# Kernel tuning notes

Hardware: AMD Instinct MI355X
Metric: run time of the kernel (lower is better)

Reference implementation:

```python
import jax, jax.numpy as jnp
import numpy as np

NUM_HEADS = 8
KEY_SIZE = 64
VALUE_SIZE = 64
NUM_GROUPS = 3 * NUM_HEADS  # 24
C = NUM_HEADS * (2 * KEY_SIZE + VALUE_SIZE)  # 1536
EPS = 1e-5


def setup_inputs() -> dict:
    key = jax.random.key(0)
    k1, k2, k3 = jax.random.split(key, 3)
    x = jax.random.normal(k1, (8, C, 32, 32), dtype=jnp.float32)
    # GroupNorm affine params (torch default ones/zeros, perturbed for non-trivial grads)
    gn_weight = 1.0 + 0.1 * jax.random.normal(k2, (C,), dtype=jnp.float32)
    gn_bias = 0.1 * jax.random.normal(k3, (C,), dtype=jnp.float32)
    return {"x": x, "gn_weight": gn_weight, "gn_bias": gn_bias}


def _group_norm(x, weight, bias):
    B, Cc, H, W = x.shape
    xg = x.reshape(B, NUM_GROUPS, -1)  # [B, G, (C/G)*H*W]
    mean = jnp.mean(xg, axis=-1, keepdims=True)
    var = jnp.var(xg, axis=-1, keepdims=True)
    xn = ((xg - mean) * jax.lax.rsqrt(var + EPS)).reshape(B, Cc, H, W)
    return xn * weight[:, None, None] + bias[:, None, None]


def reference(x, gn_weight, gn_bias):
    NH, KS, VS = NUM_HEADS, KEY_SIZE, VALUE_SIZE
    B, Cc, H, W = x.shape
    xn = _group_norm(x, gn_weight, gn_bias)
    xr = xn.reshape(B, NH, 2 * KS + VS, H * W)  # [B, NH, 2KS+VS, NK]
    k = xr[:, :, :KS]            # [B, NH, KS, NK]
    q = xr[:, :, KS:2 * KS]      # [B, NH, KS, NK]
    v = xr[:, :, 2 * KS:]        # [B, NH, VS, NK]
    # saliency = q^T @ k / sqrt(KS) -> [B, NH, NKq, NKk]
    sal = jnp.einsum('bhcq,bhck->bhqk', q, k) / jnp.sqrt(jnp.float32(KS))
    mask = jax.nn.softmax(sal, axis=-1)
    # out = v @ mask^T -> [B, NH, VS, NKq]
    out = jnp.einsum('bhvk,bhqk->bhvq', v, mask)
    return out.reshape(B, NH * VS, H, W)
```

## Files before the change

kernel.cpp:

```cpp
#include <hip/hip_runtime.h>
#include <hip/hip_bf16.h>


typedef __attribute__((ext_vector_type(8))) short bf16x8;
typedef __attribute__((ext_vector_type(4))) float f32x4;
typedef __attribute__((ext_vector_type(16))) float f32x16;
typedef unsigned short u16;
typedef unsigned int u32;

#define SM_SCALE 0.18033688f
#define SM_OFF   8.0f

__device__ __forceinline__ u32 pack2(float a, float b) {
    union { float f; u32 u; } ua, ub; ua.f = a; ub.f = b;
    return __builtin_amdgcn_perm(ub.u + 0x8000u, ua.u + 0x8000u, 0x07060302u);
}
union BB { uint4 u; bf16x8 v; };

__device__ __forceinline__ float fexp2(float x) {
#if __has_builtin(__builtin_amdgcn_exp2f)
    return __builtin_amdgcn_exp2f(x);
#else
    float r; asm("v_exp_f32 %0, %1" : "=v"(r) : "v"(x)); return r;
#endif
}

__device__ __forceinline__ f32x16 zero16() {
    f32x16 z;
#pragma unroll
    for (int i = 0; i < 16; ++i) z[i] = 0.f;
    return z;
}

__device__ __forceinline__ void swap32(u32 a, u32 b, int hi, u32& ret0, u32& ret1) {
#if __has_builtin(__builtin_amdgcn_permlane32_swap)
    (void)hi;
    auto sw = __builtin_amdgcn_permlane32_swap(a, b, false, false);
    ret0 = sw[0]; ret1 = sw[1];
#else
    u32 pa = __shfl_xor(a, 32), pb = __shfl_xor(b, 32);
    ret0 = hi ? pb : a;
    ret1 = hi ? b : pa;
#endif
}

__global__ __launch_bounds__(256) void gn_partial(const float* __restrict__ x,
                                                  float* __restrict__ partials) {
    int blk = blockIdx.x;
    const float4* p = (const float4*)(x + (size_t)blk * 8192);
    int t = threadIdx.x;
    float s1a = 0.f, s2a = 0.f, s1b = 0.f, s2b = 0.f;
#pragma unroll
    for (int i = 0; i < 8; i += 2) {
        float4 va = p[t + i * 256];
        float4 vb = p[t + (i + 1) * 256];
        s1a += va.x + va.y + va.z + va.w;
        s2a += va.x*va.x + va.y*va.y + va.z*va.z + va.w*va.w;
        s1b += vb.x + vb.y + vb.z + vb.w;
        s2b += vb.x*vb.x + vb.y*vb.y + vb.z*vb.z + vb.w*vb.w;
    }
    float s1 = s1a + s1b, s2 = s2a + s2b;
    for (int off = 32; off > 0; off >>= 1) {
        s1 += __shfl_down(s1, off);
        s2 += __shfl_down(s2, off);
    }
    __shared__ float a1[4], a2[4];
    int wave = t >> 6, lane = t & 63;
    if (lane == 0) { a1[wave] = s1; a2[wave] = s2; }
    __syncthreads();
    if (t == 0) {
        partials[blk * 2 + 0] = a1[0] + a1[1] + a1[2] + a1[3];
        partials[blk * 2 + 1] = a2[0] + a2[1] + a2[2] + a2[3];
    }
}

__device__ __forceinline__ void group_stats(const float* __restrict__ partials,
                                            int bg, float& mean, float& rstd) {
    float s1 = 0.f, s2 = 0.f;
#pragma unroll
    for (int j = 0; j < 8; ++j) {
        s1 += partials[(bg * 8 + j) * 2 + 0];
        s2 += partials[(bg * 8 + j) * 2 + 1];
    }
    mean = s1 * (1.f / 65536.f);
    float var = s2 * (1.f / 65536.f) - mean * mean;
    rstd = rsqrtf(var + 1e-5f);
}

__global__ __launch_bounds__(256, 2) void attn_fused(
    const float* __restrict__ x, const float* __restrict__ gamma,
    const float* __restrict__ beta, const float* __restrict__ partials,
    float* __restrict__ out)
{
    const int bid = blockIdx.x;
    const int qt = bid >> 6;
    const int pair = bid & 63;
    const int b = pair >> 3, h = pair & 7;
    const float* xb = x + (size_t)b * 1536 * 1024;
    const int tid = threadIdx.x;
    const int w2 = tid >> 6;
    const int lane = tid & 63;
    const int li = lane & 31;
    const int hi = lane >> 5;

    float ms[3], rs[3];
    group_stats(partials, b * 24 + 3 * h + 0, ms[0], rs[0]);
    group_stats(partials, b * 24 + 3 * h + 1, ms[1], rs[1]);
    group_stats(partials, b * 24 + 3 * h + 2, ms[2], rs[2]);

    __shared__ uint4 KT[2][512];
    __shared__ uint4 VT[2][512];

    const int sr = tid & 63;
    const int cc0 = tid >> 6;
    const int kx = sr & 7;
    const int kidx0 = sr * 8 + (cc0 ^ kx);
    const int kidx1 = sr * 8 + ((cc0 + 4) ^ kx);
    const int vidx0 = sr * 8 + ((cc0 * 2) ^ kx);
    const int vidx1 = sr * 8 + ((cc0 * 2 + 1) ^ kx);

    const float* kbase = xb + (size_t)(h * 192) * 1024 + sr;
    const float* vbase = xb + (size_t)(h * 192 + 128 + sr) * 1024 + cc0 * 16;

    const int q0 = qt * 128 + w2 * 32;
    bf16x8 bq[4];
    float dqp = 0.f;
#pragma unroll
    for (int cs = 0; cs < 4; ++cs) {
        u32 qq[4];
#pragma unroll
        for (int jp = 0; jp < 4; ++jp) {
            int c0 = cs * 16 + hi * 8 + jp * 2;
            int cgq = h * 192 + 64 + c0;
            int cgk = h * 192 + c0;
            float wq0 = gamma[cgq] * rs[1],     bq0 = beta[cgq] - ms[1] * wq0;
            float wq1 = gamma[cgq + 1] * rs[1], bq1 = beta[cgq + 1] - ms[1] * wq1;
            float wk0 = gamma[cgk] * rs[0],     bk0 = beta[cgk] - ms[0] * wk0;
            float wk1 = gamma[cgk + 1] * rs[0], bk1 = beta[cgk + 1] - ms[0] * wk1;
            float a0 = xb[(size_t)cgq * 1024 + q0 + li];
            float a1 = xb[(size_t)(cgq + 1) * 1024 + q0 + li];
            float qn0 = __builtin_fmaf(a0, wq0, bq0);
            float qn1 = __builtin_fmaf(a1, wq1, bq1);
            dqp = __builtin_fmaf(bk0, qn0, dqp);
            dqp = __builtin_fmaf(bk1, qn1, dqp);
            qq[jp] = pack2(qn0 * wk0, qn1 * wk1);
        }
        BB tb; tb.u = uint4{qq[0], qq[1], qq[2], qq[3]};
        bq[cs] = tb.v;
    }
    const float dq = dqp + __shfl_xor(dqp, 32);
    const float offq = __builtin_fmaf(dq, SM_SCALE, -SM_OFF);

    f32x16 oacc[2];
    oacc[0] = zero16(); oacc[1] = zero16();
    float lsum = 0.f;

    const int x7 = li & 7;

    float rk[16], rv[16];
#define LOAD_TILE(KT_)                                                        \
    {                                                                         \
        const float* kp = kbase + (KT_) * 64;                                 \
        _Pragma("unroll")                                                     \
        for (int u = 0; u < 16; ++u) {                                        \
            int c = ((u < 8) ? cc0 : (cc0 + 4)) * 8 + (u & 7);                \
            rk[u] = kp[(size_t)c * 1024];                                     \
        }                                                                     \
        const float* vp = vbase + (KT_) * 64;                                 \
        _Pragma("unroll")                                                     \
        for (int f = 0; f < 4; ++f) {                                         \
            float4 vq = *(const float4*)(vp + f * 4);                         \
            rv[f * 4 + 0] = vq.x; rv[f * 4 + 1] = vq.y;                       \
            rv[f * 4 + 2] = vq.z; rv[f * 4 + 3] = vq.w;                       \
        }                                                                     \
    }
#define COMMIT_TILE(BUF_)                                                     \
    {                                                                         \
        uint4 ka, kc, va, vc;                                                 \
        ka.x = pack2(rk[0], rk[1]);   ka.y = pack2(rk[2], rk[3]);             \
        ka.z = pack2(rk[4], rk[5]);   ka.w = pack2(rk[6], rk[7]);             \
        kc.x = pack2(rk[8], rk[9]);   kc.y = pack2(rk[10], rk[11]);           \
        kc.z = pack2(rk[12], rk[13]); kc.w = pack2(rk[14], rk[15]);           \
        va.x = pack2(rv[0], rv[1]);   va.y = pack2(rv[2], rv[3]);             \
        va.z = pack2(rv[4], rv[5]);   va.w = pack2(rv[6], rv[7]);             \
        vc.x = pack2(rv[8], rv[9]);   vc.y = pack2(rv[10], rv[11]);           \
        vc.z = pack2(rv[12], rv[13]); vc.w = pack2(rv[14], rv[15]);           \
        KT[BUF_][kidx0] = ka; KT[BUF_][kidx1] = kc;                           \
        VT[BUF_][vidx0] = va; VT[BUF_][vidx1] = vc;                           \
    }

    LOAD_TILE(0);
    COMMIT_TILE(0);
    __syncthreads();

#pragma unroll 2
    for (int kt = 0; kt < 16; ++kt) {
        const int cur = kt & 1;
        if (kt < 15) LOAD_TILE(kt + 1);

        BB pbv[4];
#pragma unroll
        for (int kf = 0; kf < 2; ++kf) {
            bf16x8 ak[4];
#pragma unroll
            for (int cs = 0; cs < 4; ++cs)
                ak[cs] = ((const BB*)&KT[cur][(kf * 32 + li) * 8 + ((cs * 2 + hi) ^ x7)])->v;
            f32x16 acc = zero16();
            __builtin_amdgcn_s_setprio(1);
#pragma unroll
            for (int cs = 0; cs < 4; ++cs)
                acc = __builtin_amdgcn_mfma_f32_32x32x16_bf16(ak[cs], bq[cs], acc, 0, 0, 0);
            __builtin_amdgcn_s_setprio(0);
#pragma unroll
            for (int s = 0; s < 2; ++s) {
                float p0 = fexp2(__builtin_fmaf(acc[8 * s + 0], SM_SCALE, offq));
                float p1 = fexp2(__builtin_fmaf(acc[8 * s + 1], SM_SCALE, offq));
                float p2 = fexp2(__builtin_fmaf(acc[8 * s + 2], SM_SCALE, offq));
                float p3 = fexp2(__builtin_fmaf(acc[8 * s + 3], SM_SCALE, offq));
                float p4 = fexp2(__builtin_fmaf(acc[8 * s + 4], SM_SCALE, offq));
                float p5 = fexp2(__builtin_fmaf(acc[8 * s + 5], SM_SCALE, offq));
                float p6 = fexp2(__builtin_fmaf(acc[8 * s + 6], SM_SCALE, offq));
                float p7 = fexp2(__builtin_fmaf(acc[8 * s + 7], SM_SCALE, offq));
                lsum += ((p0 + p1) + (p2 + p3)) + ((p4 + p5) + (p6 + p7));
                u32 Pa = pack2(p0, p1), Pb = pack2(p2, p3);
                u32 Pc = pack2(p4, p5), Pd = pack2(p6, p7);
                u32 w0, w1, w2m, w3;
                swap32(Pa, Pc, hi, w0, w2m);
                swap32(Pb, Pd, hi, w1, w3);
                pbv[kf * 2 + s].u = uint4{w0, w1, w2m, w3};
            }
        }

#pragma unroll
        for (int vf = 0; vf < 2; ++vf) {
            bf16x8 av[4];
#pragma unroll
            for (int ks = 0; ks < 4; ++ks)
                av[ks] = ((const BB*)&VT[cur][(vf * 32 + li) * 8 + ((ks * 2 + hi) ^ x7)])->v;
            __builtin_amdgcn_s_setprio(1);
#pragma unroll
            for (int ks = 0; ks < 4; ++ks)
                oacc[vf] = __builtin_amdgcn_mfma_f32_32x32x16_bf16(av[ks], pbv[ks].v, oacc[vf], 0, 0, 0);
            __builtin_amdgcn_s_setprio(0);
        }

        if (kt < 15) COMMIT_TILE(cur ^ 1);
        __syncthreads();
    }

    lsum += __shfl_xor(lsum, 32);
    float invl = 1.f / lsum;
    float* ob = out + (size_t)pair * 65536 + q0 + li;
#pragma unroll
    for (int vf = 0; vf < 2; ++vf)
#pragma unroll
        for (int r = 0; r < 16; ++r) {
            int v = vf * 32 + (r & 3) + 8 * (r >> 2) + 4 * hi;
            int cgv = h * 192 + 128 + v;
            float wv = gamma[cgv] * rs[2];
            float bvv = beta[cgv] - ms[2] * wv;
            ob[(size_t)v * 1024] = __builtin_fmaf(oacc[vf][r] * invl, wv, bvv);
        }
}

extern "C" void kernel_launch(void* const* d_in, const int* in_sizes, int n_in,
                              void* d_out, int out_size, void* d_ws, size_t ws_size,
                              hipStream_t stream) {
    const float* x     = (const float*)d_in[0];
    const float* gamma = (const float*)d_in[1];
    const float* beta  = (const float*)d_in[2];
    float* out = (float*)d_out;

    float* partials = (float*)d_ws;

    gn_partial<<<1536, 256, 0, stream>>>(x, partials);
    attn_fused<<<512, 256, 0, stream>>>(x, gamma, beta, partials, out);
}
```

Before: 121.0 us.

## Split key range across two 256-thread groups per block and merge partial outputs

Each block now runs 512 threads as two independent 256-thread groups. Each group processes half of the 16 key tiles with its own double-buffered LDS tiles, and the partial outputs and softmax sums are combined through shared memory at the end. This doubles the waves per block to raise latency hiding, since the grid of 512 blocks gives only about two blocks per CU. The costs are an extra LDS reduction and a barrier, doubled LDS use, and block-wide __syncthreads now coupling both groups.

```diff
diff --git a/kernel.cpp b/kernel.cpp
--- a/kernel.cpp
+++ b/kernel.cpp
@@ -87,7 +87,7 @@
     rstd = rsqrtf(var + 1e-5f);
 }
 
-__global__ __launch_bounds__(256, 2) void attn_fused(
+__global__ __launch_bounds__(512, 2) void attn_fused(
     const float* __restrict__ x, const float* __restrict__ gamma,
     const float* __restrict__ beta, const float* __restrict__ partials,
     float* __restrict__ out)
@@ -98,8 +98,10 @@
     const int b = pair >> 3, h = pair & 7;
     const float* xb = x + (size_t)b * 1536 * 1024;
     const int tid = threadIdx.x;
-    const int w2 = tid >> 6;
-    const int lane = tid & 63;
+    const int wg = tid >> 8;
+    const int t = tid & 255;
+    const int w2 = t >> 6;
+    const int lane = t & 63;
     const int li = lane & 31;
     const int hi = lane >> 5;
 
@@ -108,11 +110,10 @@
     group_stats(partials, b * 24 + 3 * h + 1, ms[1], rs[1]);
     group_stats(partials, b * 24 + 3 * h + 2, ms[2], rs[2]);
 
-    __shared__ uint4 KT[2][512];
-    __shared__ uint4 VT[2][512];
-
-    const int sr = tid & 63;
-    const int cc0 = tid >> 6;
+    __shared__ uint4 TILES[2][2][2][512];
+
+    const int sr = t & 63;
+    const int cc0 = t >> 6;
     const int kx = sr & 7;
     const int kidx0 = sr * 8 + (cc0 ^ kx);
     const int kidx1 = sr * 8 + ((cc0 + 4) ^ kx);
@@ -158,15 +159,15 @@
     const int x7 = li & 7;
 
     float rk[16], rv[16];
-#define LOAD_TILE(KT_)                                                        \
+#define LOAD_TILE(KTG_)                                                       \
     {                                                                         \
-        const float* kp = kbase + (KT_) * 64;                                 \
+        const float* kp = kbase + (KTG_) * 64;                                \
         _Pragma("unroll")                                                     \
         for (int u = 0; u < 16; ++u) {                                        \
             int c = ((u < 8) ? cc0 : (cc0 + 4)) * 8 + (u & 7);                \
             rk[u] = kp[(size_t)c * 1024];                                     \
         }                                                                     \
-        const float* vp = vbase + (KT_) * 64;                                 \
+        const float* vp = vbase + (KTG_) * 64;                                \
         _Pragma("unroll")                                                     \
         for (int f = 0; f < 4; ++f) {                                         \
             float4 vq = *(const float4*)(vp + f * 4);                         \
@@ -185,18 +186,18 @@
         va.z = pack2(rv[4], rv[5]);   va.w = pack2(rv[6], rv[7]);             \
         vc.x = pack2(rv[8], rv[9]);   vc.y = pack2(rv[10], rv[11]);           \
         vc.z = pack2(rv[12], rv[13]); vc.w = pack2(rv[14], rv[15]);           \
-        KT[BUF_][kidx0] = ka; KT[BUF_][kidx1] = kc;                           \
-        VT[BUF_][vidx0] = va; VT[BUF_][vidx1] = vc;                           \
-    }
-
-    LOAD_TILE(0);
+        TILES[wg][BUF_][0][kidx0] = ka; TILES[wg][BUF_][0][kidx1] = kc;       \
+        TILES[wg][BUF_][1][vidx0] = va; TILES[wg][BUF_][1][vidx1] = vc;       \
+    }
+
+    LOAD_TILE(wg * 8);
     COMMIT_TILE(0);
     __syncthreads();
 
 #pragma unroll 2
-    for (int kt = 0; kt < 16; ++kt) {
-        const int cur = kt & 1;
-        if (kt < 15) LOAD_TILE(kt + 1);
+    for (int kt8 = 0; kt8 < 8; ++kt8) {
+        const int cur = kt8 & 1;
+        if (kt8 < 7) LOAD_TILE(wg * 8 + kt8 + 1);
 
         BB pbv[4];
 #pragma unroll
@@ -204,7 +205,7 @@
             bf16x8 ak[4];
 #pragma unroll
             for (int cs = 0; cs < 4; ++cs)
-                ak[cs] = ((const BB*)&KT[cur][(kf * 32 + li) * 8 + ((cs * 2 + hi) ^ x7)])->v;
+                ak[cs] = ((const BB*)&TILES[wg][cur][0][(kf * 32 + li) * 8 + ((cs * 2 + hi) ^ x7)])->v;
             f32x16 acc = zero16();
             __builtin_amdgcn_s_setprio(1);
 #pragma unroll
@@ -236,7 +237,7 @@
             bf16x8 av[4];
 #pragma unroll
             for (int ks = 0; ks < 4; ++ks)
-                av[ks] = ((const BB*)&VT[cur][(vf * 32 + li) * 8 + ((ks * 2 + hi) ^ x7)])->v;
+                av[ks] = ((const BB*)&TILES[wg][cur][1][(vf * 32 + li) * 8 + ((ks * 2 + hi) ^ x7)])->v;
             __builtin_amdgcn_s_setprio(1);
 #pragma unroll
             for (int ks = 0; ks < 4; ++ks)
@@ -244,23 +245,37 @@
             __builtin_amdgcn_s_setprio(0);
         }
 
-        if (kt < 15) COMMIT_TILE(cur ^ 1);
+        if (kt8 < 7) COMMIT_TILE(cur ^ 1);
         __syncthreads();
     }
 
     lsum += __shfl_xor(lsum, 32);
-    float invl = 1.f / lsum;
-    float* ob = out + (size_t)pair * 65536 + q0 + li;
-#pragma unroll
-    for (int vf = 0; vf < 2; ++vf)
-#pragma unroll
-        for (int r = 0; r < 16; ++r) {
-            int v = vf * 32 + (r & 3) + 8 * (r >> 2) + 4 * hi;
-            int cgv = h * 192 + 128 + v;
-            float wv = gamma[cgv] * rs[2];
-            float bvv = beta[cgv] - ms[2] * wv;
-            ob[(size_t)v * 1024] = __builtin_fmaf(oacc[vf][r] * invl, wv, bvv);
-        }
+    float* Osh = (float*)TILES;
+    float* lsh = Osh + 256 * 33;
+    if (wg == 1) {
+#pragma unroll
+        for (int vf = 0; vf < 2; ++vf)
+#pragma unroll
+            for (int r = 0; r < 16; ++r)
+                Osh[t * 33 + vf * 16 + r] = oacc[vf][r];
+        lsh[t] = lsum;
+    }
+    __syncthreads();
+    if (wg == 0) {
+        float invl = 1.f / (lsum + lsh[t]);
+        float* ob = out + (size_t)pair * 65536 + q0 + li;
+#pragma unroll
+        for (int vf = 0; vf < 2; ++vf)
+#pragma unroll
+            for (int r = 0; r < 16; ++r) {
+                int v = vf * 32 + (r & 3) + 8 * (r >> 2) + 4 * hi;
+                int cgv = h * 192 + 128 + v;
+                float wv = gamma[cgv] * rs[2];
+                float bvv = beta[cgv] - ms[2] * wv;
+                float o = (oacc[vf][r] + Osh[t * 33 + vf * 16 + r]) * invl;
+                ob[(size_t)v * 1024] = __builtin_fmaf(o, wv, bvv);
+            }
+    }
 }
 
 extern "C" void kernel_launch(void* const* d_in, const int* in_sizes, int n_in,
@@ -274,5 +289,5 @@
     float* partials = (float*)d_ws;
 
     gn_partial<<<1536, 256, 0, stream>>>(x, partials);
-    attn_fused<<<512, 256, 0, stream>>>(x, gamma, beta, partials, out);
-}
+    attn_fused<<<512, 512, 0, stream>>>(x, gamma, beta, partials, out);
+}
```

Measured after the change: 132.1 us. +9.2%, slower.

## Split key range across two blocks and merge partial outputs in separate kernel

Applied to the files above, without the earlier changes.

Each attention block now processes only half of the key tiles, doubling the grid, and writes unnormalized scaled partial outputs and partial softmax sums to workspace. A new merge kernel adds the two halves, divides by the combined sum, and adds the GroupNorm bias term. This aims to increase parallelism and latency hiding, at the cost of extra global memory traffic for partials and an additional kernel launch.

```diff
diff --git a/kernel.cpp b/kernel.cpp
--- a/kernel.cpp
+++ b/kernel.cpp
@@ -90,11 +90,14 @@
 __global__ __launch_bounds__(256, 2) void attn_fused(
     const float* __restrict__ x, const float* __restrict__ gamma,
     const float* __restrict__ beta, const float* __restrict__ partials,
-    float* __restrict__ out)
+    float* __restrict__ Opart, float* __restrict__ lpart,
+    float* __restrict__ bvtab)
 {
     const int bid = blockIdx.x;
-    const int qt = bid >> 6;
     const int pair = bid & 63;
+    const int qh = bid >> 6;
+    const int qt = qh & 7;
+    const int ha = qh >> 3;
     const int b = pair >> 3, h = pair & 7;
     const float* xb = x + (size_t)b * 1536 * 1024;
     const int tid = threadIdx.x;
@@ -189,14 +192,14 @@
         VT[BUF_][vidx0] = va; VT[BUF_][vidx1] = vc;                           \
     }
 
-    LOAD_TILE(0);
+    LOAD_TILE(ha * 8);
     COMMIT_TILE(0);
     __syncthreads();
 
 #pragma unroll 2
-    for (int kt = 0; kt < 16; ++kt) {
-        const int cur = kt & 1;
-        if (kt < 15) LOAD_TILE(kt + 1);
+    for (int kt8 = 0; kt8 < 8; ++kt8) {
+        const int cur = kt8 & 1;
+        if (kt8 < 7) LOAD_TILE(ha * 8 + kt8 + 1);
 
         BB pbv[4];
 #pragma unroll
@@ -244,23 +247,53 @@
             __builtin_amdgcn_s_setprio(0);
         }
 
-        if (kt < 15) COMMIT_TILE(cur ^ 1);
+        if (kt8 < 7) COMMIT_TILE(cur ^ 1);
         __syncthreads();
     }
 
     lsum += __shfl_xor(lsum, 32);
-    float invl = 1.f / lsum;
-    float* ob = out + (size_t)pair * 65536 + q0 + li;
+    float* ob = Opart + (size_t)(ha * 64 + pair) * 65536 + q0 + li;
 #pragma unroll
     for (int vf = 0; vf < 2; ++vf)
 #pragma unroll
         for (int r = 0; r < 16; ++r) {
             int v = vf * 32 + (r & 3) + 8 * (r >> 2) + 4 * hi;
-            int cgv = h * 192 + 128 + v;
-            float wv = gamma[cgv] * rs[2];
-            float bvv = beta[cgv] - ms[2] * wv;
-            ob[(size_t)v * 1024] = __builtin_fmaf(oacc[vf][r] * invl, wv, bvv);
+            float wv = gamma[h * 192 + 128 + v] * rs[2];
+            ob[(size_t)v * 1024] = oacc[vf][r] * wv;
         }
+    if (hi == 0)
+        lpart[(size_t)(ha * 64 + pair) * 1024 + q0 + li] = lsum;
+    if (ha == 0 && tid < 64) {
+        int cgv = h * 192 + 128 + tid;
+        float wv = gamma[cgv] * rs[2];
+        bvtab[pair * 64 + tid] = beta[cgv] - ms[2] * wv;
+    }
+}
+
+__global__ __launch_bounds__(256) void merge_halves(
+    const float* __restrict__ Opart, const float* __restrict__ lpart,
+    const float* __restrict__ bvtab, float* __restrict__ out)
+{
+#pragma unroll
+    for (int i = 0; i < 8; ++i) {
+        int idx4 = blockIdx.x * 2048 + i * 256 + threadIdx.x;
+        size_t f = (size_t)idx4 * 4;
+        int pair = (int)(f >> 16);
+        int rem = (int)(f & 65535);
+        int q = rem & 1023;
+        int v = rem >> 10;
+        float4 a = *(const float4*)(Opart + (size_t)pair * 65536 + rem);
+        float4 b2 = *(const float4*)(Opart + (size_t)(64 + pair) * 65536 + rem);
+        float4 la = *(const float4*)(lpart + (size_t)pair * 1024 + q);
+        float4 lb = *(const float4*)(lpart + (size_t)(64 + pair) * 1024 + q);
+        float bvv = bvtab[pair * 64 + v];
+        float4 o;
+        o.x = (a.x + b2.x) / (la.x + lb.x) + bvv;
+        o.y = (a.y + b2.y) / (la.y + lb.y) + bvv;
+        o.z = (a.z + b2.z) / (la.z + lb.z) + bvv;
+        o.w = (a.w + b2.w) / (la.w + lb.w) + bvv;
+        *(float4*)(out + f) = o;
+    }
 }
 
 extern "C" void kernel_launch(void* const* d_in, const int* in_sizes, int n_in,
@@ -272,7 +305,11 @@
     float* out = (float*)d_out;
 
     float* partials = (float*)d_ws;
+    float* Opart = (float*)((char*)d_ws + 32768);
+    float* lpart = Opart + (size_t)2 * 64 * 65536;
+    float* bvtab = lpart + (size_t)2 * 64 * 1024;
 
     gn_partial<<<1536, 256, 0, stream>>>(x, partials);
-    attn_fused<<<512, 256, 0, stream>>>(x, gamma, beta, partials, out);
-}
+    attn_fused<<<1024, 256, 0, stream>>>(x, gamma, beta, partials, Opart, lpart, bvtab);
+    merge_halves<<<512, 256, 0, stream>>>(Opart, lpart, bvtab, out);
+}
```

Result: slower. 134.7 us (+11.3%).

## Use 512-thread blocks so eight waves share each staged K/V tile

Applied to the files above, without the earlier changes.

Each block now has eight waves and covers 256 queries instead of four waves and 128 queries, and the grid is halved. The block stages every K/V tile into LDS once for all eight waves, which halves total global K/V reads and halves the per-thread load and pack work. The K and V loading is remapped so that each thread loads and commits one 8-element chunk of each. The tighter launch bound (512 threads, 2 blocks) lowers the register budget per thread, which may cause spills. With one block per CU there is also less room to hide latency across blocks.

```diff
diff --git a/kernel.cpp b/kernel.cpp
--- a/kernel.cpp
+++ b/kernel.cpp
@@ -87,7 +87,7 @@
     rstd = rsqrtf(var + 1e-5f);
 }
 
-__global__ __launch_bounds__(256, 2) void attn_fused(
+__global__ __launch_bounds__(512, 2) void attn_fused(
     const float* __restrict__ x, const float* __restrict__ gamma,
     const float* __restrict__ beta, const float* __restrict__ partials,
     float* __restrict__ out)
@@ -111,18 +111,17 @@
     __shared__ uint4 KT[2][512];
     __shared__ uint4 VT[2][512];
 
-    const int sr = tid & 63;
-    const int cc0 = tid >> 6;
-    const int kx = sr & 7;
-    const int kidx0 = sr * 8 + (cc0 ^ kx);
-    const int kidx1 = sr * 8 + ((cc0 + 4) ^ kx);
-    const int vidx0 = sr * 8 + ((cc0 * 2) ^ kx);
-    const int vidx1 = sr * 8 + ((cc0 * 2 + 1) ^ kx);
-
-    const float* kbase = xb + (size_t)(h * 192) * 1024 + sr;
-    const float* vbase = xb + (size_t)(h * 192 + 128 + sr) * 1024 + cc0 * 16;
-
-    const int q0 = qt * 128 + w2 * 32;
+    const int sr  = tid & 63;
+    const int kcc = tid >> 6;
+    const int kidx = sr * 8 + (kcc ^ (sr & 7));
+    const int vc  = tid >> 3;
+    const int vs8 = (tid & 7) * 8;
+    const int vidx = vc * 8 + ((tid & 7) ^ (vc & 7));
+
+    const float* kbase = xb + (size_t)(h * 192 + kcc * 8) * 1024 + sr;
+    const float* vbase = xb + (size_t)(h * 192 + 128 + vc) * 1024 + vs8;
+
+    const int q0 = qt * 256 + w2 * 32;
     bf16x8 bq[4];
     float dqp = 0.f;
 #pragma unroll
@@ -157,36 +156,26 @@
 
     const int x7 = li & 7;
 
-    float rk[16], rv[16];
+    float rk[8], rv[8];
 #define LOAD_TILE(KT_)                                                        \
     {                                                                         \
         const float* kp = kbase + (KT_) * 64;                                 \
         _Pragma("unroll")                                                     \
-        for (int u = 0; u < 16; ++u) {                                        \
-            int c = ((u < 8) ? cc0 : (cc0 + 4)) * 8 + (u & 7);                \
-            rk[u] = kp[(size_t)c * 1024];                                     \
-        }                                                                     \
+        for (int u = 0; u < 8; ++u) rk[u] = kp[(size_t)u * 1024];             \
         const float* vp = vbase + (KT_) * 64;                                 \
-        _Pragma("unroll")                                                     \
-        for (int f = 0; f < 4; ++f) {                                         \
-            float4 vq = *(const float4*)(vp + f * 4);                         \
-            rv[f * 4 + 0] = vq.x; rv[f * 4 + 1] = vq.y;                       \
-            rv[f * 4 + 2] = vq.z; rv[f * 4 + 3] = vq.w;                       \
-        }                                                                     \
+        float4 v0 = *(const float4*)(vp);                                     \
+        float4 v1 = *(const float4*)(vp + 4);                                 \
+        rv[0] = v0.x; rv[1] = v0.y; rv[2] = v0.z; rv[3] = v0.w;               \
+        rv[4] = v1.x; rv[5] = v1.y; rv[6] = v1.z; rv[7] = v1.w;               \
     }
 #define COMMIT_TILE(BUF_)                                                     \
     {                                                                         \
-        uint4 ka, kc, va, vc;                                                 \
-        ka.x = pack2(rk[0], rk[1]);   ka.y = pack2(rk[2], rk[3]);             \
-        ka.z = pack2(rk[4], rk[5]);   ka.w = pack2(rk[6], rk[7]);             \
-        kc.x = pack2(rk[8], rk[9]);   kc.y = pack2(rk[10], rk[11]);           \
-        kc.z = pack2(rk[12], rk[13]); kc.w = pack2(rk[14], rk[15]);           \
-        va.x = pack2(rv[0], rv[1]);   va.y = pack2(rv[2], rv[3]);             \
-        va.z = pack2(rv[4], rv[5]);   va.w = pack2(rv[6], rv[7]);             \
-        vc.x = pack2(rv[8], rv[9]);   vc.y = pack2(rv[10], rv[11]);           \
-        vc.z = pack2(rv[12], rv[13]); vc.w = pack2(rv[14], rv[15]);           \
-        KT[BUF_][kidx0] = ka; KT[BUF_][kidx1] = kc;                           \
-        VT[BUF_][vidx0] = va; VT[BUF_][vidx1] = vc;                           \
+        uint4 ka, va;                                                         \
+        ka.x = pack2(rk[0], rk[1]); ka.y = pack2(rk[2], rk[3]);               \
+        ka.z = pack2(rk[4], rk[5]); ka.w = pack2(rk[6], rk[7]);               \
+        va.x = pack2(rv[0], rv[1]); va.y = pack2(rv[2], rv[3]);               \
+        va.z = pack2(rv[4], rv[5]); va.w = pack2(rv[6], rv[7]);               \
+        KT[BUF_][kidx] = ka; VT[BUF_][vidx] = va;                             \
     }
 
     LOAD_TILE(0);
@@ -274,5 +263,5 @@
     float* partials = (float*)d_ws;
 
     gn_partial<<<1536, 256, 0, stream>>>(x, partials);
-    attn_fused<<<512, 256, 0, stream>>>(x, gamma, beta, partials, out);
-}
+    attn_fused<<<256, 512, 0, stream>>>(x, gamma, beta, partials, out);
+}
```

New measurement: 116.9 us. -3.3%, faster.
